# Kernel tuning notes

Hardware: AMD Instinct MI355X
Metric: run time of the kernel (lower is better)

## Reference

```python
import jax, jax.numpy as jnp
import numpy as np

N_NODES = 50000
N_EDGES = 800000
NUM_RELS = 16
IN_DIM, H_DIM, OUT_DIM = 128, 128, 64


def setup_inputs() -> dict:
    key = jax.random.key(0)
    ks = jax.random.split(key, 7)
    feat = jax.random.normal(ks[0], (N_NODES, IN_DIM), dtype=jnp.float32)
    norm = jax.random.uniform(ks[1], (N_EDGES, 1), dtype=jnp.float32)
    bound1 = 1.0 / np.sqrt(IN_DIM)
    bound2 = 1.0 / np.sqrt(H_DIM)
    W1 = jax.random.uniform(ks[2], (NUM_RELS, IN_DIM, H_DIM), dtype=jnp.float32, minval=-bound1, maxval=bound1)
    W2 = jax.random.uniform(ks[3], (NUM_RELS, H_DIM, OUT_DIM), dtype=jnp.float32, minval=-bound2, maxval=bound2)
    src = jax.random.randint(ks[4], (N_EDGES,), 0, N_NODES, dtype=jnp.int32)
    dst = jax.random.randint(ks[5], (N_EDGES,), 0, N_NODES, dtype=jnp.int32)
    etypes = jax.random.randint(ks[6], (N_EDGES,), 0, NUM_RELS, dtype=jnp.int32)
    return {"feat": feat, "norm": norm, "W1": W1, "W2": W2, "src": src, "dst": dst, "etypes": etypes}


def _rgcn_layer(h, W, src, dst, etypes, norm, num_nodes):
    # Transform every node by every relation weight (dense batched GEMM),
    # then gather the (src, etype) slice per edge: identical math to
    # gather_mm(h[src], W, idx_b=etypes) since matmul commutes with gather.
    t = jnp.einsum('ni,rio->nro', h, W)          # [N, R, O]
    msg = t[src, etypes] * norm                  # [E, O]
    return jax.ops.segment_sum(msg, dst, num_segments=num_nodes)  # sum-aggregate


def reference(feat, norm, W1, W2, src, dst, etypes):
    n = feat.shape[0]
    h = jax.nn.relu(_rgcn_layer(feat, W1, src, dst, etypes, norm, n))
    out = _rgcn_layer(h, W2, src, dst, etypes, norm, n)
    return out
```

## Files before the change

kernel.cpp:

```cpp
#include <hip/hip_runtime.h>


#define R_NUM 16

typedef __attribute__((ext_vector_type(8))) short bf16x8;
typedef __attribute__((ext_vector_type(4))) float f32x4;

__device__ __forceinline__ float bf2f(unsigned short u) {
    unsigned int x = ((unsigned int)u) << 16;
    return __builtin_bit_cast(float, x);
}
__device__ __forceinline__ unsigned short f2bf(float f) {
    unsigned int x = __builtin_bit_cast(unsigned int, f);
    x += 0x7FFFu + ((x >> 16) & 1u);
    return (unsigned short)(x >> 16);
}
__device__ __forceinline__ unsigned pack2(float a, float b) {
    return (unsigned)f2bf(a) | ((unsigned)f2bf(b) << 16);
}
__device__ __forceinline__ float lo16(unsigned v) { return bf2f((unsigned short)(v & 0xFFFF)); }
__device__ __forceinline__ float hi16(unsigned v) { return bf2f((unsigned short)(v >> 16)); }

__global__ void detect_dtype(const unsigned short* __restrict__ raw, int* flag) {
    __shared__ int tot;
    if (threadIdx.x == 0) tot = 0;
    __syncthreads();
    int c = 0;
    for (int i = threadIdx.x; i < 4096; i += 256) {
        unsigned short u = raw[2 * i];
        int e = (u >> 7) & 0xFF;
        if (e >= 113 && e <= 134) c++;
    }
    atomicAdd(&tot, c);
    __syncthreads();
    if (threadIdx.x == 0) *flag = (tot > 2048) ? 1 : 0;
}

__global__ void transpose_both(const void* __restrict__ W1, const void* __restrict__ W2,
                               unsigned short* __restrict__ w1t, unsigned short* __restrict__ w2t,
                               const int* __restrict__ flagp) {
    const int flag = *flagp;
    const int n1 = R_NUM * 128 * 128;
    const int n2 = R_NUM * 128 * 64;
    int idx = blockIdx.x * 256 + threadIdx.x;
    if (idx < n1) {
        int k = idx % 128, o = (idx / 128) % 128, r = idx / (128 * 128);
        int iin = (r * 128 + k) * 128 + o;
        float v = flag ? bf2f(((const unsigned short*)W1)[iin]) : ((const float*)W1)[iin];
        w1t[idx] = f2bf(v);
    } else if (idx < n1 + n2) {
        int j = idx - n1;
        int k = j % 128, o = (j / 128) % 64, r = j / (128 * 64);
        int iin = (r * 128 + k) * 64 + o;
        float v = flag ? bf2f(((const unsigned short*)W2)[iin]) : ((const float*)W2)[iin];
        w2t[j] = f2bf(v);
    }
}

template <int NOUT, int AMODE>
__global__ __launch_bounds__(256, 3) void gemm_all(const void* __restrict__ Asrc,
                                                   const unsigned short* __restrict__ Wt,
                                                   unsigned short* __restrict__ T, int nnodes,
                                                   const int* __restrict__ flagp) {
    constexpr int LDA = 136;
    constexpr int NTC = NOUT / 64;
    __shared__ unsigned short lA[64 * LDA];
    __shared__ unsigned short lB[NOUT * LDA];
    const int tid = threadIdx.x;
    const int node0 = blockIdx.x * 64;
    const int flag = (AMODE == 0) ? *flagp : 1;

    for (int i = tid; i < 64 * 16; i += 256) {
        int row = i >> 4, seg = i & 15;
        int node = node0 + row;
        uint4 v = make_uint4(0u, 0u, 0u, 0u);
        if (node < nnodes) {
            if (AMODE == 2 || flag) {
                v = *(const uint4*)((const unsigned short*)Asrc + (size_t)node * 128 + seg * 8);
            } else {
                const float* p = (const float*)Asrc + (size_t)node * 128 + seg * 8;
                float4 f0 = ((const float4*)p)[0];
                float4 f1 = ((const float4*)p)[1];
                v.x = pack2(f0.x, f0.y);
                v.y = pack2(f0.z, f0.w);
                v.z = pack2(f1.x, f1.y);
                v.w = pack2(f1.z, f1.w);
            }
        }
        *(uint4*)(lA + row * LDA + seg * 8) = v;
    }

    auto stageB = [&](int rel) {
        for (int i = tid; i < NOUT * 16; i += 256) {
            int o = i >> 4, seg = i & 15;
            *(uint4*)(lB + o * LDA + seg * 8) =
                *(const uint4*)(Wt + ((size_t)rel * NOUT + o) * 128 + seg * 8);
        }
    };
    stageB(0);
    __syncthreads();

    const int w = tid >> 6, lane = tid & 63;
    const int quad = lane >> 4, mr = lane & 15;

    bf16x8 afr[16];
#pragma unroll
    for (int mt = 0; mt < 4; mt++)
#pragma unroll
        for (int kk = 0; kk < 4; kk++)
            afr[mt * 4 + kk] = *(const bf16x8*)(lA + (mt * 16 + mr) * LDA + kk * 32 + quad * 8);

    constexpr int SEGS = NOUT / 8;
    constexpr int SPT = 64 * SEGS / 256;

    for (int rel = 0; rel < R_NUM; rel++) {
        f32x4 acc[4][NTC];
#pragma unroll
        for (int mt = 0; mt < 4; mt++)
#pragma unroll
            for (int c = 0; c < NTC; c++) acc[mt][c] = 0.f;

#pragma unroll
        for (int kk = 0; kk < 4; kk++) {
#pragma unroll
            for (int c = 0; c < NTC; c++) {
                bf16x8 b = *(const bf16x8*)(lB + (c * 64 + w * 16 + mr) * LDA + kk * 32 + quad * 8);
#pragma unroll
                for (int mt = 0; mt < 4; mt++)
                    acc[mt][c] = __builtin_amdgcn_mfma_f32_16x16x32_bf16(b, afr[mt * 4 + kk],
                                                                         acc[mt][c], 0, 0, 0);
            }
        }
        __syncthreads();

        if (rel + 1 < R_NUM) stageB(rel + 1);
#pragma unroll
        for (int mt = 0; mt < 4; mt++)
#pragma unroll
            for (int c = 0; c < NTC; c++) {
                uint2 pv;
                pv.x = pack2(acc[mt][c][0], acc[mt][c][1]);
                pv.y = pack2(acc[mt][c][2], acc[mt][c][3]);
                *(uint2*)(lA + (mt * 16 + mr) * LDA + c * 64 + w * 16 + quad * 4) = pv;
            }
        __syncthreads();

#pragma unroll
        for (int it = 0; it < SPT; it++) {
            int i = it * 256 + tid;
            int row = i / SEGS, seg = i % SEGS;
            int node = node0 + row;
            if (node < nnodes)
                *(uint4*)(T + ((size_t)rel * nnodes + node) * NOUT + seg * 8) =
                    *(const uint4*)(lA + row * LDA + seg * 8);
        }
    }
}

__global__ void hist_dst(const int* __restrict__ dst, int* __restrict__ counts, int nedges) {
    int e = blockIdx.x * 256 + threadIdx.x;
    if (e < nedges) atomicAdd(&counts[dst[e]], 1);
}

__global__ __launch_bounds__(256) void scan_phase1(const int* __restrict__ counts,
                                                   int* __restrict__ blocksums, int n) {
    __shared__ int red[256];
    int base = blockIdx.x * 1024 + threadIdx.x * 4;
    int s = 0;
#pragma unroll
    for (int j = 0; j < 4; j++) {
        int idx = base + j;
        if (idx < n) s += counts[idx];
    }
    red[threadIdx.x] = s;
    __syncthreads();
    for (int d = 128; d > 0; d >>= 1) {
        if (threadIdx.x < d) red[threadIdx.x] += red[threadIdx.x + d];
        __syncthreads();
    }
    if (threadIdx.x == 0) blocksums[blockIdx.x] = red[0];
}

__global__ __launch_bounds__(1024) void scan_phase2(const int* __restrict__ blocksums,
                                                    int* __restrict__ blockoff, int nb) {
    __shared__ int arr[1024];
    int t = threadIdx.x;
    arr[t] = (t < nb) ? blocksums[t] : 0;
    __syncthreads();
    for (int d = 1; d < 1024; d <<= 1) {
        int v = (t >= d) ? arr[t - d] : 0;
        __syncthreads();
        arr[t] += v;
        __syncthreads();
    }
    if (t < nb) blockoff[t] = (t == 0) ? 0 : arr[t - 1];
}

__global__ __launch_bounds__(256) void scan_phase3(const int* __restrict__ counts,
                                                   const int* __restrict__ blockoff,
                                                   int* __restrict__ offsets,
                                                   int* __restrict__ cursor, int n) {
    __shared__ int tsum[256];
    int base = blockIdx.x * 1024 + threadIdx.x * 4;
    int c[4];
    int s = 0;
#pragma unroll
    for (int j = 0; j < 4; j++) {
        int idx = base + j;
        c[j] = (idx < n) ? counts[idx] : 0;
        s += c[j];
    }
    tsum[threadIdx.x] = s;
    __syncthreads();
    for (int d = 1; d < 256; d <<= 1) {
        int v = (threadIdx.x >= d) ? tsum[threadIdx.x - d] : 0;
        __syncthreads();
        tsum[threadIdx.x] += v;
        __syncthreads();
    }
    int run = blockoff[blockIdx.x] + ((threadIdx.x == 0) ? 0 : tsum[threadIdx.x - 1]);
#pragma unroll
    for (int j = 0; j < 4; j++) {
        int idx = base + j;
        if (idx < n) {
            offsets[idx] = run;
            cursor[idx] = run;
            if (idx == n - 1) offsets[n] = run + c[j];
            run += c[j];
        }
    }
}

__global__ void fill_payload(const int* __restrict__ src, const int* __restrict__ dst,
                             const int* __restrict__ et, const void* __restrict__ nrm,
                             const int* __restrict__ flagp, int* __restrict__ cursor,
                             uint2* __restrict__ payload, int nedges) {
    int e = blockIdx.x * 256 + threadIdx.x;
    if (e >= nedges) return;
    int flag = *flagp;
    float nm = flag ? bf2f(((const unsigned short*)nrm)[e]) : ((const float*)nrm)[e];
    int pos = atomicAdd(&cursor[dst[e]], 1);
    uint2 pl;
    pl.x = ((unsigned)src[e] << 4) | (unsigned)(et[e] & 15);
    pl.y = __builtin_bit_cast(unsigned, nm);
    payload[pos] = pl;
}

template <int NOUT, int OUTMODE>
__global__ __launch_bounds__(256) void gather_seg(const unsigned short* __restrict__ T,
                                                  const int* __restrict__ offsets,
                                                  const uint2* __restrict__ payload,
                                                  void* __restrict__ out, int nnodes,
                                                  const int* __restrict__ flagp) {
    constexpr int SUBW = NOUT / 2;
    const int lane = threadIdx.x & 63;
    const int ll = lane & (SUBW - 1);
    const int dpb = 256 / SUBW;
    const int dst = blockIdx.x * dpb + threadIdx.x / SUBW;
    if (dst >= nnodes) return;
    const int base = lane & ~(SUBW - 1);
    const int beg = offsets[dst], end = offsets[dst + 1];
    float ax = 0.f, ay = 0.f;

    auto rowp = [&](unsigned key) {
        return (const unsigned*)(T + ((size_t)(key & 15) * nnodes + (key >> 4)) * NOUT);
    };

    for (int i = beg; i < end; i += SUBW) {
        int cnt = min(SUBW, end - i);
        uint2 pl = make_uint2(0u, 0u);
        if (ll < cnt) pl = payload[i + ll];
        int j = 0;
        for (; j + 4 <= cnt; j += 4) {
            unsigned k0 = (unsigned)__shfl((int)pl.x, base + j);
            unsigned k1 = (unsigned)__shfl((int)pl.x, base + j + 1);
            unsigned k2 = (unsigned)__shfl((int)pl.x, base + j + 2);
            unsigned k3 = (unsigned)__shfl((int)pl.x, base + j + 3);
            float n0 = __builtin_bit_cast(float, (unsigned)__shfl((int)pl.y, base + j));
            float n1 = __builtin_bit_cast(float, (unsigned)__shfl((int)pl.y, base + j + 1));
            float n2 = __builtin_bit_cast(float, (unsigned)__shfl((int)pl.y, base + j + 2));
            float n3 = __builtin_bit_cast(float, (unsigned)__shfl((int)pl.y, base + j + 3));
            unsigned v0 = rowp(k0)[ll];
            unsigned v1 = rowp(k1)[ll];
            unsigned v2 = rowp(k2)[ll];
            unsigned v3 = rowp(k3)[ll];
            ax = fmaf(lo16(v0), n0, ax); ay = fmaf(hi16(v0), n0, ay);
            ax = fmaf(lo16(v1), n1, ax); ay = fmaf(hi16(v1), n1, ay);
            ax = fmaf(lo16(v2), n2, ax); ay = fmaf(hi16(v2), n2, ay);
            ax = fmaf(lo16(v3), n3, ax); ay = fmaf(hi16(v3), n3, ay);
        }
        for (; j < cnt; j++) {
            unsigned k = (unsigned)__shfl((int)pl.x, base + j);
            float nm = __builtin_bit_cast(float, (unsigned)__shfl((int)pl.y, base + j));
            unsigned v = rowp(k)[ll];
            ax = fmaf(lo16(v), nm, ax);
            ay = fmaf(hi16(v), nm, ay);
        }
    }
    if (OUTMODE == 0) {
        ((unsigned*)out)[(size_t)dst * SUBW + ll] = pack2(fmaxf(ax, 0.f), fmaxf(ay, 0.f));
    } else {
        if (*flagp) {
            ((unsigned*)out)[(size_t)dst * SUBW + ll] = pack2(ax, ay);
        } else {
            float2 v;
            v.x = ax; v.y = ay;
            ((float2*)out)[(size_t)dst * SUBW + ll] = v;
        }
    }
}

template <int NOUT, int AMODE>
__global__ __launch_bounds__(256) void gemm_rel(const void* __restrict__ Asrc,
                                                const unsigned short* __restrict__ Wt,
                                                unsigned short* __restrict__ T, int nnodes,
                                                int rbase, const int* __restrict__ flagp) {
    constexpr int LDA = 136;
    __shared__ unsigned short lA[64 * LDA];
    __shared__ unsigned short lB[NOUT * LDA];
    const int tid = threadIdx.x;
    const int node0 = blockIdx.x * 64;
    const int rel = rbase + blockIdx.y;
    const int Gr = gridDim.y;
    const int flag = (AMODE == 0) ? *flagp : 1;

    for (int i = tid; i < 64 * 16; i += 256) {
        int row = i >> 4, seg = i & 15;
        int node = node0 + row;
        uint4 v = make_uint4(0u, 0u, 0u, 0u);
        if (node < nnodes) {
            if (AMODE == 1) {
                const float* p = (const float*)Asrc + (size_t)node * 128 + seg * 8;
                float4 f0 = ((const float4*)p)[0];
                float4 f1 = ((const float4*)p)[1];
                v.x = pack2(fmaxf(f0.x, 0.f), fmaxf(f0.y, 0.f));
                v.y = pack2(fmaxf(f0.z, 0.f), fmaxf(f0.w, 0.f));
                v.z = pack2(fmaxf(f1.x, 0.f), fmaxf(f1.y, 0.f));
                v.w = pack2(fmaxf(f1.z, 0.f), fmaxf(f1.w, 0.f));
            } else if (flag) {
                v = *(const uint4*)((const unsigned short*)Asrc + (size_t)node * 128 + seg * 8);
            } else {
                const float* p = (const float*)Asrc + (size_t)node * 128 + seg * 8;
                float4 f0 = ((const float4*)p)[0];
                float4 f1 = ((const float4*)p)[1];
                v.x = pack2(f0.x, f0.y);
                v.y = pack2(f0.z, f0.w);
                v.z = pack2(f1.x, f1.y);
                v.w = pack2(f1.z, f1.w);
            }
        }
        *(uint4*)(lA + row * LDA + seg * 8) = v;
    }
    for (int i = tid; i < NOUT * 16; i += 256) {
        int o = i >> 4, seg = i & 15;
        *(uint4*)(lB + o * LDA + seg * 8) =
            *(const uint4*)(Wt + ((size_t)rel * NOUT + o) * 128 + seg * 8);
    }
    __syncthreads();

    const int w = tid >> 6, lane = tid & 63;
    const int quad = lane >> 4, mr = lane & 15;
    constexpr int NT = NOUT / 16;
    f32x4 acc[NT];
#pragma unroll
    for (int t = 0; t < NT; t++) acc[t] = 0.f;
    const unsigned short* pa = lA + (w * 16 + mr) * LDA + quad * 8;
    const unsigned short* pb = lB + mr * LDA + quad * 8;
#pragma unroll
    for (int kk = 0; kk < 4; kk++) {
        bf16x8 a = *(const bf16x8*)(pa + kk * 32);
#pragma unroll
        for (int nt = 0; nt < NT; nt++) {
            bf16x8 b = *(const bf16x8*)(pb + nt * 16 * LDA + kk * 32);
            acc[nt] = __builtin_amdgcn_mfma_f32_16x16x32_bf16(a, b, acc[nt], 0, 0, 0);
        }
    }
#pragma unroll
    for (int nt = 0; nt < NT; nt++)
#pragma unroll
        for (int reg = 0; reg < 4; reg++) {
            int node = node0 + w * 16 + quad * 4 + reg;
            if (node < nnodes)
                T[((size_t)node * Gr + blockIdx.y) * NOUT + nt * 16 + mr] = f2bf(acc[nt][reg]);
        }
}

template <int NOUT>
__global__ void scatter_k(const unsigned short* __restrict__ T, int Gr, int rbase,
                          const void* __restrict__ nrm, const int* __restrict__ flagp,
                          const int* __restrict__ src, const int* __restrict__ dst,
                          const int* __restrict__ et, float* __restrict__ accum, int nedges) {
    constexpr int LPE = NOUT / 2;
    const int flag = *flagp;
    const int epb = 256 / LPE;
    const int sub = threadIdx.x % LPE;
    const int slot = threadIdx.x / LPE;
    for (int e = blockIdx.x * epb + slot; e < nedges; e += gridDim.x * epb) {
        int g = et[e] - rbase;
        if (g < 0 || g >= Gr) continue;
        int s = src[e], d = dst[e];
        float nm = flag ? bf2f(((const unsigned short*)nrm)[e]) : ((const float*)nrm)[e];
        unsigned pv = ((const unsigned*)(T + ((size_t)s * Gr + g) * NOUT))[sub];
        float* p = accum + (size_t)d * NOUT + sub * 2;
        unsafeAtomicAdd(p, lo16(pv) * nm);
        unsafeAtomicAdd(p + 1, hi16(pv) * nm);
    }
}

__global__ void write_out(const float* __restrict__ acc, void* __restrict__ dout, int n,
                          const int* __restrict__ flagp) {
    int flag = *flagp;
    int i = blockIdx.x * 256 + threadIdx.x;
    if (i >= n) return;
    float v = acc[i];
    if (flag) ((unsigned short*)dout)[i] = f2bf(v);
    else      ((float*)dout)[i] = v;
}

extern "C" void kernel_launch(void* const* d_in, const int* in_sizes, int n_in,
                              void* d_out, int out_size, void* d_ws, size_t ws_size,
                              hipStream_t stream) {
    const void* feat = d_in[0];
    const void* norm = d_in[1];
    const void* W1 = d_in[2];
    const void* W2 = d_in[3];
    const int* src = (const int*)d_in[4];
    const int* dst = (const int*)d_in[5];
    const int* et  = (const int*)d_in[6];

    const int nnodes = in_sizes[0] / 128;
    const int nedges = in_sizes[1];

    char* ws = (char*)d_ws;
    size_t off = 0;
    auto alloc = [&](size_t bytes) { size_t o = off; off += (bytes + 255) & ~255ULL; return o; };
    size_t off_flag = alloc(4);
    size_t off_w1t  = alloc((size_t)R_NUM * 128 * 128 * 2);
    size_t off_w2t  = alloc((size_t)R_NUM * 64 * 128 * 2);

    int* flagp = (int*)(ws + off_flag);
    unsigned short* w1t = (unsigned short*)(ws + off_w1t);
    unsigned short* w2t = (unsigned short*)(ws + off_w2t);

    size_t f_off = off;
    auto falloc = [&](size_t bytes) { size_t o = f_off; f_off += (bytes + 255) & ~255ULL; return o; };
    size_t off_offs = falloc((size_t)(nnodes + 1) * 4);
    size_t off_curs = falloc((size_t)nnodes * 4);
    size_t off_cnt  = falloc((size_t)nnodes * 4);
    size_t off_bsum = falloc(1024 * 4);
    size_t off_boff = falloc(1024 * 4);
    size_t off_pay  = falloc((size_t)nedges * 8);
    size_t off_hbf  = falloc((size_t)nnodes * 128 * 2);
    size_t off_t    = falloc((size_t)nnodes * R_NUM * 128 * 2);
    const int nb = (nnodes + 1023) / 1024;
    bool fast = (f_off <= ws_size) && (nb <= 1024);

    const int gx = (nnodes + 63) / 64;
    const int ntr = R_NUM * 128 * 128 + R_NUM * 128 * 64;

    detect_dtype<<<1, 256, 0, stream>>>((const unsigned short*)feat, flagp);
    transpose_both<<<(ntr + 255) / 256, 256, 0, stream>>>(W1, W2, w1t, w2t, flagp);

    if (fast) {
        int* offs = (int*)(ws + off_offs);
        int* curs = (int*)(ws + off_curs);
        int* cnt  = (int*)(ws + off_cnt);
        int* bsum = (int*)(ws + off_bsum);
        int* boff = (int*)(ws + off_boff);
        uint2* pay = (uint2*)(ws + off_pay);
        unsigned short* hbf = (unsigned short*)(ws + off_hbf);
        unsigned short* t = (unsigned short*)(ws + off_t);

        hipMemsetAsync(cnt, 0, (size_t)nnodes * 4, stream);
        hist_dst<<<(nedges + 255) / 256, 256, 0, stream>>>(dst, cnt, nedges);
        scan_phase1<<<nb, 256, 0, stream>>>(cnt, bsum, nnodes);
        scan_phase2<<<1, 1024, 0, stream>>>(bsum, boff, nb);
        scan_phase3<<<nb, 256, 0, stream>>>(cnt, boff, offs, curs, nnodes);
        fill_payload<<<(nedges + 255) / 256, 256, 0, stream>>>(src, dst, et, norm, flagp,
                                                               curs, pay, nedges);

        gemm_all<128, 0><<<gx, 256, 0, stream>>>(feat, w1t, t, nnodes, flagp);
        gather_seg<128, 0><<<(nnodes + 3) / 4, 256, 0, stream>>>(t, offs, pay, hbf, nnodes, flagp);
        gemm_all<64, 2><<<gx, 256, 0, stream>>>(hbf, w2t, t, nnodes, flagp);
        gather_seg<64, 1><<<(nnodes + 7) / 8, 256, 0, stream>>>(t, offs, pay, d_out, nnodes, flagp);
        return;
    }

    size_t off_hpre = alloc((size_t)nnodes * 128 * 4);
    size_t off_oacc = alloc((size_t)nnodes * 64 * 4);
    size_t t_cap = (ws_size > off) ? (ws_size - off) : 0;
    auto pick_gr = [&](int ncol) {
        int gr = 0;
        for (int g = 16; g >= 1; g >>= 1)
            if ((size_t)nnodes * g * ncol * 2 <= t_cap) { gr = g; break; }
        return gr;
    };
    int Gr1 = pick_gr(128);
    int Gr2 = pick_gr(64);
    if (Gr1 < 1 || Gr2 < 1) {
        hipMemsetAsync(d_out, 0x42, (size_t)out_size * 2, stream);
        return;
    }
    float* hpre = (float*)(ws + off_hpre);
    float* oacc = (float*)(ws + off_oacc);
    unsigned short* t = (unsigned short*)(ws + off);

    hipMemsetAsync(hpre, 0, (size_t)nnodes * 128 * 4, stream);
    hipMemsetAsync(oacc, 0, (size_t)nnodes * 64 * 4, stream);
    for (int rb = 0; rb < R_NUM; rb += Gr1) {
        gemm_rel<128, 0><<<dim3(gx, Gr1), 256, 0, stream>>>(feat, w1t, t, nnodes, rb, flagp);
        scatter_k<128><<<4096, 256, 0, stream>>>(t, Gr1, rb, norm, flagp, src, dst, et, hpre, nedges);
    }
    for (int rb = 0; rb < R_NUM; rb += Gr2) {
        gemm_rel<64, 1><<<dim3(gx, Gr2), 256, 0, stream>>>(hpre, w2t, t, nnodes, rb, flagp);
        scatter_k<64><<<4096, 256, 0, stream>>>(t, Gr2, rb, norm, flagp, src, dst, et, oacc, nedges);
    }
    int nout = nnodes * 64;
    write_out<<<(nout + 255) / 256, 256, 0, stream>>>(oacc, d_out, nout, flagp);
}
```

Measured before the change: 393.5 us.

## Split per-node GEMM into one block per (node tile, relation) with pre-converted bf16 input

The GEMM kernel used to loop over all 16 relations inside each block, keeping the node tile in registers and staging each relation's weights serially between barriers. Now each block handles a single (64-node tile, relation) pair, which gives 16x more blocks and removes the serial per-relation barrier chain. A separate to_bf16 kernel converts the input features once so the GEMM reads only bf16. The cost is that the A tile is reloaded from global memory 16 times, plus an extra launch and pass over the features.

```diff
diff --git a/kernel.cpp b/kernel.cpp
--- a/kernel.cpp
+++ b/kernel.cpp
@@ -57,103 +57,98 @@
     }
 }
 
-template <int NOUT, int AMODE>
-__global__ __launch_bounds__(256, 3) void gemm_all(const void* __restrict__ Asrc,
-                                                   const unsigned short* __restrict__ Wt,
-                                                   unsigned short* __restrict__ T, int nnodes,
-                                                   const int* __restrict__ flagp) {
+__global__ void to_bf16(const void* __restrict__ in, unsigned short* __restrict__ out, int n8,
+                        const int* __restrict__ flagp) {
+    int i = blockIdx.x * 256 + threadIdx.x;
+    if (i >= n8) return;
+    uint4 v;
+    if (*flagp) {
+        v = ((const uint4*)in)[i];
+    } else {
+        const float4* p = (const float4*)in + (size_t)i * 2;
+        float4 f0 = p[0];
+        float4 f1 = p[1];
+        v.x = pack2(f0.x, f0.y);
+        v.y = pack2(f0.z, f0.w);
+        v.z = pack2(f1.x, f1.y);
+        v.w = pack2(f1.z, f1.w);
+    }
+    ((uint4*)out)[i] = v;
+}
+
+template <int NOUT>
+__global__ __launch_bounds__(256, 3) void gemm_plane(const unsigned short* __restrict__ A,
+                                                     const unsigned short* __restrict__ Wt,
+                                                     unsigned short* __restrict__ T, int nnodes) {
     constexpr int LDA = 136;
     constexpr int NTC = NOUT / 64;
     __shared__ unsigned short lA[64 * LDA];
     __shared__ unsigned short lB[NOUT * LDA];
     const int tid = threadIdx.x;
-    const int node0 = blockIdx.x * 64;
-    const int flag = (AMODE == 0) ? *flagp : 1;
+    const int rel = blockIdx.x & 15;
+    const int node0 = (blockIdx.x >> 4) * 64;
 
     for (int i = tid; i < 64 * 16; i += 256) {
         int row = i >> 4, seg = i & 15;
         int node = node0 + row;
         uint4 v = make_uint4(0u, 0u, 0u, 0u);
-        if (node < nnodes) {
-            if (AMODE == 2 || flag) {
-                v = *(const uint4*)((const unsigned short*)Asrc + (size_t)node * 128 + seg * 8);
-            } else {
-                const float* p = (const float*)Asrc + (size_t)node * 128 + seg * 8;
-                float4 f0 = ((const float4*)p)[0];
-                float4 f1 = ((const float4*)p)[1];
-                v.x = pack2(f0.x, f0.y);
-                v.y = pack2(f0.z, f0.w);
-                v.z = pack2(f1.x, f1.y);
-                v.w = pack2(f1.z, f1.w);
-            }
-        }
+        if (node < nnodes) v = *(const uint4*)(A + (size_t)node * 128 + seg * 8);
         *(uint4*)(lA + row * LDA + seg * 8) = v;
     }
-
-    auto stageB = [&](int rel) {
-        for (int i = tid; i < NOUT * 16; i += 256) {
-            int o = i >> 4, seg = i & 15;
-            *(uint4*)(lB + o * LDA + seg * 8) =
-                *(const uint4*)(Wt + ((size_t)rel * NOUT + o) * 128 + seg * 8);
-        }
-    };
-    stageB(0);
+    for (int i = tid; i < NOUT * 16; i += 256) {
+        int o = i >> 4, seg = i & 15;
+        *(uint4*)(lB + o * LDA + seg * 8) =
+            *(const uint4*)(Wt + ((size_t)rel * NOUT + o) * 128 + seg * 8);
+    }
     __syncthreads();
 
     const int w = tid >> 6, lane = tid & 63;
     const int quad = lane >> 4, mr = lane & 15;
 
-    bf16x8 afr[16];
+    f32x4 acc[4][NTC];
 #pragma unroll
     for (int mt = 0; mt < 4; mt++)
 #pragma unroll
-        for (int kk = 0; kk < 4; kk++)
-            afr[mt * 4 + kk] = *(const bf16x8*)(lA + (mt * 16 + mr) * LDA + kk * 32 + quad * 8);
+        for (int c = 0; c < NTC; c++) acc[mt][c] = 0.f;
+
+#pragma unroll
+    for (int kk = 0; kk < 4; kk++) {
+        bf16x8 a[4];
+#pragma unroll
+        for (int mt = 0; mt < 4; mt++)
+            a[mt] = *(const bf16x8*)(lA + (mt * 16 + mr) * LDA + kk * 32 + quad * 8);
+#pragma unroll
+        for (int c = 0; c < NTC; c++) {
+            bf16x8 b = *(const bf16x8*)(lB + (c * 64 + w * 16 + mr) * LDA + kk * 32 + quad * 8);
+#pragma unroll
+            for (int mt = 0; mt < 4; mt++)
+                acc[mt][c] =
+                    __builtin_amdgcn_mfma_f32_16x16x32_bf16(b, a[mt], acc[mt][c], 0, 0, 0);
+        }
+    }
+    __syncthreads();
+
+#pragma unroll
+    for (int mt = 0; mt < 4; mt++)
+#pragma unroll
+        for (int c = 0; c < NTC; c++) {
+            uint2 pv;
+            pv.x = pack2(acc[mt][c][0], acc[mt][c][1]);
+            pv.y = pack2(acc[mt][c][2], acc[mt][c][3]);
+            *(uint2*)(lA + (mt * 16 + mr) * LDA + c * 64 + w * 16 + quad * 4) = pv;
+        }
+    __syncthreads();
 
     constexpr int SEGS = NOUT / 8;
     constexpr int SPT = 64 * SEGS / 256;
-
-    for (int rel = 0; rel < R_NUM; rel++) {
-        f32x4 acc[4][NTC];
-#pragma unroll
-        for (int mt = 0; mt < 4; mt++)
-#pragma unroll
-            for (int c = 0; c < NTC; c++) acc[mt][c] = 0.f;
-
-#pragma unroll
-        for (int kk = 0; kk < 4; kk++) {
-#pragma unroll
-            for (int c = 0; c < NTC; c++) {
-                bf16x8 b = *(const bf16x8*)(lB + (c * 64 + w * 16 + mr) * LDA + kk * 32 + quad * 8);
-#pragma unroll
-                for (int mt = 0; mt < 4; mt++)
-                    acc[mt][c] = __builtin_amdgcn_mfma_f32_16x16x32_bf16(b, afr[mt * 4 + kk],
-                                                                         acc[mt][c], 0, 0, 0);
-            }
-        }
-        __syncthreads();
-
-        if (rel + 1 < R_NUM) stageB(rel + 1);
-#pragma unroll
-        for (int mt = 0; mt < 4; mt++)
-#pragma unroll
-            for (int c = 0; c < NTC; c++) {
-                uint2 pv;
-                pv.x = pack2(acc[mt][c][0], acc[mt][c][1]);
-                pv.y = pack2(acc[mt][c][2], acc[mt][c][3]);
-                *(uint2*)(lA + (mt * 16 + mr) * LDA + c * 64 + w * 16 + quad * 4) = pv;
-            }
-        __syncthreads();
-
-#pragma unroll
-        for (int it = 0; it < SPT; it++) {
-            int i = it * 256 + tid;
-            int row = i / SEGS, seg = i % SEGS;
-            int node = node0 + row;
-            if (node < nnodes)
-                *(uint4*)(T + ((size_t)rel * nnodes + node) * NOUT + seg * 8) =
-                    *(const uint4*)(lA + row * LDA + seg * 8);
-        }
+#pragma unroll
+    for (int it = 0; it < SPT; it++) {
+        int i = it * 256 + tid;
+        int row = i / SEGS, seg = i % SEGS;
+        int node = node0 + row;
+        if (node < nnodes)
+            *(uint4*)(T + ((size_t)rel * nnodes + node) * NOUT + seg * 8) =
+                *(const uint4*)(lA + row * LDA + seg * 8);
     }
 }
 
@@ -450,7 +445,7 @@
     size_t off_bsum = falloc(1024 * 4);
     size_t off_boff = falloc(1024 * 4);
     size_t off_pay  = falloc((size_t)nedges * 8);
-    size_t off_hbf  = falloc((size_t)nnodes * 128 * 2);
+    size_t off_nbf  = falloc((size_t)nnodes * 128 * 2);
     size_t off_t    = falloc((size_t)nnodes * R_NUM * 128 * 2);
     const int nb = (nnodes + 1023) / 1024;
     bool fast = (f_off <= ws_size) && (nb <= 1024);
@@ -468,7 +463,7 @@
         int* bsum = (int*)(ws + off_bsum);
         int* boff = (int*)(ws + off_boff);
         uint2* pay = (uint2*)(ws + off_pay);
-        unsigned short* hbf = (unsigned short*)(ws + off_hbf);
+        unsigned short* nbf = (unsigned short*)(ws + off_nbf);
         unsigned short* t = (unsigned short*)(ws + off_t);
 
         hipMemsetAsync(cnt, 0, (size_t)nnodes * 4, stream);
@@ -479,9 +474,12 @@
         fill_payload<<<(nedges + 255) / 256, 256, 0, stream>>>(src, dst, et, norm, flagp,
                                                                curs, pay, nedges);
 
-        gemm_all<128, 0><<<gx, 256, 0, stream>>>(feat, w1t, t, nnodes, flagp);
-        gather_seg<128, 0><<<(nnodes + 3) / 4, 256, 0, stream>>>(t, offs, pay, hbf, nnodes, flagp);
-        gemm_all<64, 2><<<gx, 256, 0, stream>>>(hbf, w2t, t, nnodes, flagp);
+        const int n8 = nnodes * 16;
+        to_bf16<<<(n8 + 255) / 256, 256, 0, stream>>>(feat, nbf, n8, flagp);
+
+        gemm_plane<128><<<gx * 16, 256, 0, stream>>>(nbf, w1t, t, nnodes);
+        gather_seg<128, 0><<<(nnodes + 3) / 4, 256, 0, stream>>>(t, offs, pay, nbf, nnodes, flagp);
+        gemm_plane<64><<<gx * 16, 256, 0, stream>>>(nbf, w2t, t, nnodes);
         gather_seg<64, 1><<<(nnodes + 7) / 8, 256, 0, stream>>>(t, offs, pay, d_out, nnodes, flagp);
         return;
     }
```

After: 384.6 us. -2.3%, faster.
